# Optimization experiments

Hardware: AMD Instinct MI355X
Metric: run time of the kernel (lower is better)

The kernel has to match this reference:

```python
import jax, jax.numpy as jnp
import numpy as np

DN = ('NHWC', 'HWIO', 'NHWC')
EPS = 1e-8
BN_EPS = 1e-3
ROUT_ITERS = 3


def _bn(x, p, axis):
    # p: [4, C] rows = gamma, beta, moving_mean, moving_var (inference-mode BN)
    shp = [1] * x.ndim
    shp[axis % x.ndim] = x.shape[axis % x.ndim]
    g, b, m, v = [p[i].reshape(shp) for i in range(4)]
    return (x - m) * jax.lax.rsqrt(v + BN_EPS) * g + b


def _conv(x, w, b, stride, pad):
    return jax.lax.conv_general_dilated(x, w, (stride, stride), pad, dimension_numbers=DN) + b


def _patches(x, k, s):
    # x: [B, H, W, ...] -> [B, Ho, Wo, k*k, ...] (static k*k strided slices, no big gathers)
    Ho = (x.shape[1] - k) // s + 1
    Wo = (x.shape[2] - k) // s + 1
    sl = [x[:, i:i + s * (Ho - 1) + 1:s, j:j + s * (Wo - 1) + 1:s]
          for i in range(k) for j in range(k)]
    return jnp.stack(sl, axis=3)


def _em_routing(votes, a_in, beta_a, beta_u, iters=ROUT_ITERS):
    # votes: [..., Nin, Nout, D], a_in: [..., Nin]; Hinton matrix-capsule EM routing
    Nout = votes.shape[-2]
    R = jnp.full(votes.shape[:-1], 1.0 / Nout, votes.dtype)  # [..., Nin, Nout]
    a_ex = a_in[..., None]
    for i in range(iters):
        lam = 0.01 * (i + 1)  # inverse-temperature schedule
        Ra = R * a_ex                                             # [..., Nin, Nout]
        Rs = Ra.sum(-2) + EPS                                     # [..., Nout]
        mu = jnp.einsum('...no,...nod->...od', Ra, votes) / Rs[..., None]
        diff2 = (votes - mu[..., None, :, :]) ** 2                # [..., Nin, Nout, D]
        sig2 = jnp.einsum('...no,...nod->...od', Ra, diff2) / Rs[..., None] + EPS
        cost = (beta_u[:, None] + 0.5 * jnp.log(sig2)) * Rs[..., None]
        a_out = jax.nn.sigmoid(lam * (beta_a - cost.sum(-1)))     # [..., Nout]
        if i < iters - 1:
            logp = -0.5 * jnp.sum(diff2 / sig2[..., None, :, :]
                                  + jnp.log(2.0 * jnp.pi * sig2)[..., None, :, :], axis=-1)
            R = jax.nn.softmax(jnp.log(a_out + EPS)[..., None, :] + logp, axis=-1)
    return mu, a_out


def _convcaps(pose, a, W, beta_a, beta_u, k=3, s=2):
    # pose: [B,H,W,C,4,4], a: [B,H,W,C]; W: [k*k*C, Cout, 4, 4]
    pp = _patches(pose, k, s)                  # [B,Ho,Wo,k*k,C,4,4]
    B, Ho, Wo = pp.shape[:3]
    pp = pp.reshape(B, Ho, Wo, -1, 4, 4)       # [B,Ho,Wo,Nin,4,4]
    ap = _patches(a, k, s).reshape(B, Ho, Wo, -1)
    Cout = W.shape[1]
    votes = jnp.einsum('bhwnij,nojk->bhwnoik', pp, W).reshape(B, Ho, Wo, pp.shape[3], Cout, 16)
    mu, a_out = _em_routing(votes, ap, beta_a, beta_u)
    return mu.reshape(B, Ho, Wo, Cout, 4, 4), a_out


def reference(x, conv_w, conv_b, bn1, prim_pose_w, prim_pose_b, prim_act_w, prim_act_b,
              bn2, cc1_w, cc1_ba, cc1_bu, bn3, cc2_w, cc2_ba, cc2_bu, bn4,
              dc_w, dc_ba, dc_bu, dec_w1, dec_b1, dec_w2, dec_b2, dec_w3, dec_b3):
    h = jax.nn.relu(_conv(x, conv_w, conv_b, 2, 'SAME'))          # conv1 + relu
    h = _bn(h, bn1, -1)
    pose = _conv(h, prim_pose_w, prim_pose_b, 2, 'VALID')         # PrimaryCaps pose conv
    B, H, W, _ = pose.shape
    pose = pose.reshape(B, H, W, 32, 4, 4)
    a = jax.nn.sigmoid(_conv(h, prim_act_w, prim_act_b, 2, 'VALID'))
    pose = _bn(pose, bn2, -3)
    pose, a = _convcaps(pose, a, cc1_w, cc1_ba, cc1_bu)
    pose = _bn(pose, bn3, -3)
    pose, a = _convcaps(pose, a, cc2_w, cc2_ba, cc2_bu)
    pose = _bn(pose, bn4, -3)
    # DenseCaps: flatten spatial grid of capsules
    pflat = pose.reshape(B, -1, 4, 4)                             # [B, 1152, 4, 4]
    aflat = a.reshape(B, -1)
    votes = jnp.einsum('bnij,nojk->bnoik', pflat, dc_w).reshape(B, pflat.shape[1], dc_w.shape[1], 16)
    mu, a_out = _em_routing(votes, aflat, dc_ba, dc_bu)           # mu: [B, 32, 16]
    dec_in = mu.reshape(B, -1)                                    # [B, 512]
    h = jax.nn.relu(dec_in @ dec_w1 + dec_b1)
    h = jax.nn.relu(h @ dec_w2 + dec_b2)
    return h @ dec_w3 + dec_b3


def _bn_params(k, C):
    k1, k2, k3, k4 = jax.random.split(k, 4)
    return jnp.stack([1.0 + 0.05 * jax.random.normal(k1, (C,)),
                      0.05 * jax.random.normal(k2, (C,)),
                      0.01 * jax.random.normal(k3, (C,)),
                      1.0 + 0.1 * jax.random.uniform(k4, (C,))]).astype(jnp.float32)


def setup_inputs() -> dict:
    key = jax.random.key(0)
    ks = jax.random.split(key, 24)
    B, HW, NV = 2, 128, 8192
    n = lambda k, s, sc: (sc * jax.random.normal(k, s)).astype(jnp.float32)
    return {
        'x': n(ks[0], (B, HW, HW, 3), 1.0),
        'conv_w': n(ks[1], (11, 11, 3, 96), 0.05), 'conv_b': n(ks[2], (96,), 0.05),
        'bn1': _bn_params(ks[3], 96),
        'prim_pose_w': n(ks[4], (9, 9, 96, 32 * 16), 0.05), 'prim_pose_b': n(ks[5], (32 * 16,), 0.05),
        'prim_act_w': n(ks[6], (9, 9, 96, 32), 0.05), 'prim_act_b': n(ks[7], (32,), 0.05),
        'bn2': _bn_params(ks[8], 32),
        'cc1_w': n(ks[9], (3 * 3 * 32, 32, 4, 4), 0.1),
        'cc1_ba': n(ks[10], (32,), 0.5), 'cc1_bu': n(ks[11], (32,), 0.5),
        'bn3': _bn_params(ks[12], 32),
        'cc2_w': n(ks[13], (3 * 3 * 32, 32, 4, 4), 0.1),
        'cc2_ba': n(ks[14], (32,), 0.5), 'cc2_bu': n(ks[15], (32,), 0.5),
        'bn4': _bn_params(ks[16], 32),
        'dc_w': n(ks[17], (6 * 6 * 32, 32, 4, 4), 0.1),
        'dc_ba': n(ks[18], (32,), 0.5), 'dc_bu': n(ks[19], (32,), 0.5),
        'dec_w1': n(ks[20], (512, 512), 0.05), 'dec_b1': jnp.zeros((512,), jnp.float32),
        'dec_w2': n(ks[21], (512, 1024), 0.05), 'dec_b2': jnp.zeros((1024,), jnp.float32),
        'dec_w3': n(ks[22], (1024, NV), 0.02), 'dec_b3': jnp.zeros((NV,), jnp.float32),
    }
```

## Files before the change

### kernel.cpp

```cpp
#include <hip/hip_runtime.h>
#include <hip/hip_bf16.h>

#define EPSR 1e-8f
#define BNEPS 1e-3f
#define LOG2PI 1.8378770664093453f

#define O_H      0
#define O_POSE2  786432
#define O_ACT2   1589248
#define O_POSE3  1639424
#define O_ACT3   1812480
#define O_POSE4  1823296
#define O_ACT4   1860160
#define O_DECIN  1862464
#define O_H1     1863488
#define O_H2     1864512
#define O_PART   1866560
#define O_DSTAT  0
#define O_DCOMB  32768

__global__ __launch_bounds__(256) void conv1_k(
    const float* __restrict__ x, const float* __restrict__ w,
    const float* __restrict__ bias, const float* __restrict__ bn1,
    float* __restrict__ h)
{
  int t = blockIdx.x * 256 + threadIdx.x;
  int c = t % 96; int px = t / 96;
  int ox = px & 63; int r = px >> 6; int oy = r & 63; int b = r >> 6;
  float acc = 0.f;
  int iy0 = 2*oy - 4, ix0 = 2*ox - 4;
  for (int ky = 0; ky < 11; ++ky) {
    int iy = iy0 + ky;
    if ((unsigned)iy > 127u) continue;
    const float* xrow = x + (size_t)((b*128 + iy)*128)*3;
    const float* wrow = w + (ky*11*3)*96 + c;
    for (int kx = 0; kx < 11; ++kx) {
      int ix = ix0 + kx;
      if ((unsigned)ix > 127u) continue;
      const float* xp = xrow + ix*3;
      const float* wp = wrow + kx*3*96;
      acc = fmaf(xp[0], wp[0],   acc);
      acc = fmaf(xp[1], wp[96],  acc);
      acc = fmaf(xp[2], wp[192], acc);
    }
  }
  acc += bias[c];
  acc = fmaxf(acc, 0.f);
  float g = bn1[c], be = bn1[96+c], mm = bn1[192+c], vv = bn1[288+c];
  h[t] = (acc - mm) * (g * rsqrtf(vv + BNEPS)) + be;
}

__global__ __launch_bounds__(256) void zero_raw(float* __restrict__ pose2, float* __restrict__ act2)
{
  int t = blockIdx.x * 256 + threadIdx.x;
  if (t < 802816) pose2[t] = 0.f;
  else act2[t - 802816] = 0.f;
}

__global__ __launch_bounds__(256) void conv2_gemm_ks(
    const float* __restrict__ h,
    const float* __restrict__ pw, const float* __restrict__ aw,
    float* __restrict__ pose2r, float* __restrict__ act2r)
{
  __shared__ float As[2][16][68];
  __shared__ float Bs[2][16][68];
  const int tid = threadIdx.x;
  const int mb = blockIdx.x, nb = blockIdx.y, z = blockIdx.z;
  const int m0 = mb * 64;
  const float* Bp; int ldB, n0;
  if (nb < 8) { Bp = pw; ldB = 512; n0 = nb * 64; } else { Bp = aw; ldB = 32; n0 = 0; }

  const int a_ml = tid & 63, a_cig = tid >> 6;
  const int am = m0 + a_ml;
  const bool am_ok = am < 1568;
  int ab_ = am / 784; int ayx = am - ab_*784;
  int aoy = ayx / 28, aox = ayx - aoy*28;
  if (!am_ok) { ab_ = 0; aoy = 0; aox = 0; }
  const float* a_base = h + (size_t)((ab_*64 + 2*aoy)*64 + 2*aox)*96 + a_cig*4;

  const int b_kk = tid >> 4, b_ng = tid & 15;
  const int b_col = b_ng * 4;
  const bool b_ok = b_col < ldB;

  const int tm = (tid & 15) * 4, tn = (tid >> 4) * 4;
  float acc[4][4] = {{0}};

  auto kidx = [](int kt, int& ky, int& kx, int& ci0) {
    int cig = kt % 6; int r = kt / 6; kx = r % 9; ky = r / 9; ci0 = cig * 16;
  };
  auto ldAv = [&](int ky, int kx, int ci0) -> float4 {
    if (!am_ok) return make_float4(0,0,0,0);
    return *(const float4*)(a_base + (ky*64 + kx)*96 + ci0);
  };
  auto ldBv = [&](int kt) -> float4 {
    if (!b_ok) return make_float4(0,0,0,0);
    return *(const float4*)(Bp + (size_t)(kt*16 + b_kk) * ldB + n0 + b_col);
  };
  auto wrAv = [&](float4 v, int buf) {
    As[buf][a_cig*4+0][a_ml] = v.x;
    As[buf][a_cig*4+1][a_ml] = v.y;
    As[buf][a_cig*4+2][a_ml] = v.z;
    As[buf][a_cig*4+3][a_ml] = v.w;
  };
  auto wrBv = [&](float4 v, int buf) {
    *(float4*)&Bs[buf][b_kk][b_col] = v;
  };

  const int kt0 = z * 81;
  {
    int ky, kx, ci0; kidx(kt0, ky, kx, ci0);
    wrAv(ldAv(ky, kx, ci0), 0); wrBv(ldBv(kt0), 0);
  }
  __syncthreads();

  for (int i = 0; i < 81; ++i) {
    int cur = i & 1;
    bool st = i < 80;
    float4 va, vb;
    if (st) {
      int ky, kx, ci0; kidx(kt0 + i + 1, ky, kx, ci0);
      va = ldAv(ky, kx, ci0);
      vb = ldBv(kt0 + i + 1);
    }
    #pragma unroll
    for (int kk = 0; kk < 16; ++kk) {
      float4 av = *(const float4*)&As[cur][kk][tm];
      float4 bv = *(const float4*)&Bs[cur][kk][tn];
      float aa[4] = {av.x, av.y, av.z, av.w};
      float bb4[4] = {bv.x, bv.y, bv.z, bv.w};
      #pragma unroll
      for (int ii = 0; ii < 4; ++ii)
        #pragma unroll
        for (int jj = 0; jj < 4; ++jj)
          acc[ii][jj] = fmaf(aa[ii], bb4[jj], acc[ii][jj]);
    }
    if (st) { wrAv(va, cur ^ 1); wrBv(vb, cur ^ 1); }
    __syncthreads();
  }

  #pragma unroll
  for (int i = 0; i < 4; ++i) {
    int m = m0 + tm + i;
    if (m >= 1568) break;
    #pragma unroll
    for (int j = 0; j < 4; ++j) {
      int nl = tn + j;
      if (nb < 8) {
        atomicAdd(&pose2r[(size_t)m*512 + n0 + nl], acc[i][j]);
      } else if (nl < 32) {
        atomicAdd(&act2r[(size_t)m*32 + nl], acc[i][j]);
      }
    }
  }
}

__global__ __launch_bounds__(256) void conv2_epi(
    const float* __restrict__ pb, const float* __restrict__ ab,
    const float* __restrict__ bn2,
    float* __restrict__ pose2, float* __restrict__ act2)
{
  int t = blockIdx.x * 256 + threadIdx.x;
  if (t < 802816) {
    int n = t & 511;
    float val = pose2[t] + pb[n];
    int caps = n >> 4;
    float g = bn2[caps], be = bn2[32+caps], mm = bn2[64+caps], vv = bn2[96+caps];
    pose2[t] = (val - mm) * (g * rsqrtf(vv + BNEPS)) + be;
  } else {
    int t2 = t - 802816;
    int nl = t2 & 31;
    float val = act2[t2] + ab[nl];
    act2[t2] = 1.f / (1.f + expf(-val));
  }
}

template<int NIN, int NWAVES, bool CONV>
__global__ __launch_bounds__(NWAVES*64) void routing_k(
    const float* __restrict__ pose_in, const float* __restrict__ act_in,
    const float* __restrict__ Wv,
    const float* __restrict__ ba, const float* __restrict__ bu,
    const float* __restrict__ bn,
    float* __restrict__ pose_out, float* __restrict__ act_out,
    int Hin, int Win, int Wout)
{
  constexpr int NT  = NWAVES * 64;
  constexpr int NPW = NIN / NWAVES;
  __shared__ float s1s[NWAVES][32*17];
  __shared__ float s2s[NWAVES][32*17];
  __shared__ float rsP[NWAVES][32];
  __shared__ float muS[32*17], isgS[32*17], lgS[32*17];
  __shared__ float laS[32], lsS[32], aoS[32], RsS[32], S0S[32];

  const int tid = threadIdx.x;
  const int wv = tid >> 6, lane = tid & 63;
  const int o = lane & 31, half = lane >> 5;

  int bb = 0, oy = 0, ox = 0;
  if (CONV) {
    int px = blockIdx.x;
    ox = px % Wout; int t2 = px / Wout; oy = t2 % Wout; bb = t2 / Wout;
  } else {
    bb = blockIdx.x;
  }

  float mur[8], isgr[8], lar = 0.f, lsr = 0.f;
  #pragma unroll
  for (int i = 0; i < 8; ++i) { mur[i] = 0.f; isgr[i] = 0.f; }

  for (int p = 0; p < 3; ++p) {
    float lam = 0.01f * (float)(p + 1);
    float s1r[8] = {0,0,0,0,0,0,0,0};
    float s2r[8] = {0,0,0,0,0,0,0,0};
    float rsr = 0.f;

    for (int it = 0; it < NPW; ++it) {
      int n = wv * NPW + it;
      const float* wp = Wv + (size_t)(n*32 + o) * 16;
      float4 w0 = *(const float4*)(wp);
      float4 w1 = *(const float4*)(wp + 4);
      float4 w2 = *(const float4*)(wp + 8);
      float4 w3 = *(const float4*)(wp + 12);
      const float* pp; float an;
      if (CONV) {
        int c = n & 31, kk = n >> 5;
        int ki = kk / 3, kj = kk - ki*3;
        int pix = (bb*Hin + 2*oy + ki)*Win + 2*ox + kj;
        pp = pose_in + (size_t)(pix*32 + c) * 16;
        an = act_in[pix*32 + c];
      } else {
        pp = pose_in + (size_t)(bb*NIN + n) * 16;
        an = act_in[bb*NIN + n];
      }
      float4 p0 = *(const float4*)(pp + half*8);
      float4 p1 = *(const float4*)(pp + half*8 + 4);
      float v[8];
      v[0] = fmaf(p0.x,w0.x, fmaf(p0.y,w1.x, fmaf(p0.z,w2.x, p0.w*w3.x)));
      v[1] = fmaf(p0.x,w0.y, fmaf(p0.y,w1.y, fmaf(p0.z,w2.y, p0.w*w3.y)));
      v[2] = fmaf(p0.x,w0.z, fmaf(p0.y,w1.z, fmaf(p0.z,w2.z, p0.w*w3.z)));
      v[3] = fmaf(p0.x,w0.w, fmaf(p0.y,w1.w, fmaf(p0.z,w2.w, p0.w*w3.w)));
      v[4] = fmaf(p1.x,w0.x, fmaf(p1.y,w1.x, fmaf(p1.z,w2.x, p1.w*w3.x)));
      v[5] = fmaf(p1.x,w0.y, fmaf(p1.y,w1.y, fmaf(p1.z,w2.y, p1.w*w3.y)));
      v[6] = fmaf(p1.x,w0.z, fmaf(p1.y,w1.z, fmaf(p1.z,w2.z, p1.w*w3.z)));
      v[7] = fmaf(p1.x,w0.w, fmaf(p1.y,w1.w, fmaf(p1.z,w2.w, p1.w*w3.w)));

      float R;
      if (p == 0) {
        R = 1.f / 32.f;
      } else {
        float t = 0.f;
        #pragma unroll
        for (int dd = 0; dd < 8; ++dd) { float df = v[dd] - mur[dd]; t = fmaf(df*df, isgr[dd], t); }
        t += __shfl_xor(t, 32, 64);
        float logit = lar - 0.5f * (t + lsr);
        float mx = logit;
        mx = fmaxf(mx, __shfl_xor(mx, 16, 64));
        mx = fmaxf(mx, __shfl_xor(mx,  8, 64));
        mx = fmaxf(mx, __shfl_xor(mx,  4, 64));
        mx = fmaxf(mx, __shfl_xor(mx,  2, 64));
        mx = fmaxf(mx, __shfl_xor(mx,  1, 64));
        float e = expf(logit - mx);
        float se = e;
        se += __shfl_xor(se, 16, 64);
        se += __shfl_xor(se,  8, 64);
        se += __shfl_xor(se,  4, 64);
        se += __shfl_xor(se,  2, 64);
        se += __shfl_xor(se,  1, 64);
        R = e / se;
      }
      float Ra = R * an;
      rsr += Ra;
      #pragma unroll
      for (int dd = 0; dd < 8; ++dd) {
        s1r[dd] = fmaf(Ra, v[dd], s1r[dd]);
        s2r[dd] = fmaf(Ra * v[dd], v[dd], s2r[dd]);
      }
    }

    #pragma unroll
    for (int dd = 0; dd < 8; ++dd) {
      s1s[wv][o*17 + half*8 + dd] = s1r[dd];
      s2s[wv][o*17 + half*8 + dd] = s2r[dd];
    }
    if (!half) rsP[wv][o] = rsr;
    __syncthreads();
    if (tid < 32) {
      float r = 0.f;
      #pragma unroll
      for (int w2 = 0; w2 < NWAVES; ++w2) r += rsP[w2][tid];
      S0S[tid] = r; RsS[tid] = r + EPSR;
    }
    __syncthreads();
    for (int idx = tid; idx < 512; idx += NT) {
      int oo = idx >> 4, d = idx & 15;
      float S1 = 0.f, S2 = 0.f;
      #pragma unroll
      for (int w2 = 0; w2 < NWAVES; ++w2) { S1 += s1s[w2][oo*17+d]; S2 += s2s[w2][oo*17+d]; }
      float Rs = RsS[oo];
      float m_ = S1 / Rs;
      float sg = (S2 - 2.f*m_*S1 + m_*m_*S0S[oo]) / Rs + EPSR;
      muS[oo*17+d]  = m_;
      isgS[oo*17+d] = 1.f / sg;
      lgS[oo*17+d]  = logf(sg);
    }
    __syncthreads();
    if (tid < 32) {
      float L = 0.f;
      #pragma unroll
      for (int d = 0; d < 16; ++d) L += lgS[tid*17 + d];
      float cost = (16.f*bu[tid] + 0.5f*L) * RsS[tid];
      float av = 1.f / (1.f + expf(-lam * (ba[tid] - cost)));
      aoS[tid] = av;
      laS[tid] = logf(av + EPSR);
      lsS[tid] = 16.f*LOG2PI + L;
    }
    __syncthreads();
    if (p < 2) {
      #pragma unroll
      for (int dd = 0; dd < 8; ++dd) {
        mur[dd]  = muS[o*17 + half*8 + dd];
        isgr[dd] = isgS[o*17 + half*8 + dd];
      }
      lar = laS[o]; lsr = lsS[o];
    }
  }

  if (CONV) {
    int pxo = (bb*Wout + oy)*Wout + ox;
    for (int idx = tid; idx < 512; idx += NT) {
      int oo = idx >> 4, d = idx & 15;
      float val = muS[oo*17 + d];
      float g = bn[oo], be = bn[32+oo], mm = bn[64+oo], vv = bn[96+oo];
      val = (val - mm) * (g * rsqrtf(vv + BNEPS)) + be;
      pose_out[(size_t)pxo*512 + idx] = val;
    }
    if (tid < 32) act_out[(size_t)pxo*32 + tid] = aoS[tid];
  } else {
    for (int idx = tid; idx < 512; idx += NT)
      pose_out[(size_t)bb*512 + idx] = muS[(idx>>4)*17 + (idx&15)];
  }
}

template<int P>
__global__ __launch_bounds__(256) void dense_stats(
    const float* __restrict__ pose_in, const float* __restrict__ act_in,
    const float* __restrict__ Wv, const float* __restrict__ comb,
    float* __restrict__ stat)
{
  __shared__ float s1s[4][32*17];
  __shared__ float s2s[4][32*17];
  __shared__ float rsP[4][32];
  const int tid = threadIdx.x;
  const int wv = tid >> 6, lane = tid & 63;
  const int o = lane & 31, half = lane >> 5;
  const int bb = blockIdx.x / 12, chunk = blockIdx.x % 12;

  float mur[8], isgr[8], lar = 0.f, lsr = 0.f;
  if (P > 0) {
    const float* cb = comb + (size_t)bb * 1088;
    #pragma unroll
    for (int dd = 0; dd < 8; ++dd) {
      mur[dd]  = cb[o*16 + half*8 + dd];
      isgr[dd] = cb[512 + o*16 + half*8 + dd];
    }
    lar = cb[1024 + o]; lsr = cb[1056 + o];
  }

  float s1r[8] = {0,0,0,0,0,0,0,0};
  float s2r[8] = {0,0,0,0,0,0,0,0};
  float rsr = 0.f;

  for (int it = 0; it < 24; ++it) {
    int n = chunk*96 + wv*24 + it;
    const float* wp = Wv + (size_t)(n*32 + o) * 16;
    float4 w0 = *(const float4*)(wp);
    float4 w1 = *(const float4*)(wp + 4);
    float4 w2 = *(const float4*)(wp + 8);
    float4 w3 = *(const float4*)(wp + 12);
    const float* pp = pose_in + (size_t)(bb*1152 + n) * 16;
    float an = act_in[bb*1152 + n];
    float4 p0 = *(const float4*)(pp + half*8);
    float4 p1 = *(const float4*)(pp + half*8 + 4);
    float v[8];
    v[0] = fmaf(p0.x,w0.x, fmaf(p0.y,w1.x, fmaf(p0.z,w2.x, p0.w*w3.x)));
    v[1] = fmaf(p0.x,w0.y, fmaf(p0.y,w1.y, fmaf(p0.z,w2.y, p0.w*w3.y)));
    v[2] = fmaf(p0.x,w0.z, fmaf(p0.y,w1.z, fmaf(p0.z,w2.z, p0.w*w3.z)));
    v[3] = fmaf(p0.x,w0.w, fmaf(p0.y,w1.w, fmaf(p0.z,w2.w, p0.w*w3.w)));
    v[4] = fmaf(p1.x,w0.x, fmaf(p1.y,w1.x, fmaf(p1.z,w2.x, p1.w*w3.x)));
    v[5] = fmaf(p1.x,w0.y, fmaf(p1.y,w1.y, fmaf(p1.z,w2.y, p1.w*w3.y)));
    v[6] = fmaf(p1.x,w0.z, fmaf(p1.y,w1.z, fmaf(p1.z,w2.z, p1.w*w3.z)));
    v[7] = fmaf(p1.x,w0.w, fmaf(p1.y,w1.w, fmaf(p1.z,w2.w, p1.w*w3.w)));

    float R;
    if (P == 0) {
      R = 1.f / 32.f;
    } else {
      float t = 0.f;
      #pragma unroll
      for (int dd = 0; dd < 8; ++dd) { float df = v[dd] - mur[dd]; t = fmaf(df*df, isgr[dd], t); }
      t += __shfl_xor(t, 32, 64);
      float logit = lar - 0.5f * (t + lsr);
      float mx = logit;
      mx = fmaxf(mx, __shfl_xor(mx, 16, 64));
      mx = fmaxf(mx, __shfl_xor(mx,  8, 64));
      mx = fmaxf(mx, __shfl_xor(mx,  4, 64));
      mx = fmaxf(mx, __shfl_xor(mx,  2, 64));
      mx = fmaxf(mx, __shfl_xor(mx,  1, 64));
      float e = expf(logit - mx);
      float se = e;
      se += __shfl_xor(se, 16, 64);
      se += __shfl_xor(se,  8, 64);
      se += __shfl_xor(se,  4, 64);
      se += __shfl_xor(se,  2, 64);
      se += __shfl_xor(se,  1, 64);
      R = e / se;
    }
    float Ra = R * an;
    rsr += Ra;
    #pragma unroll
    for (int dd = 0; dd < 8; ++dd) {
      s1r[dd] = fmaf(Ra, v[dd], s1r[dd]);
      s2r[dd] = fmaf(Ra * v[dd], v[dd], s2r[dd]);
    }
  }

  #pragma unroll
  for (int dd = 0; dd < 8; ++dd) {
    s1s[wv][o*17 + half*8 + dd] = s1r[dd];
    s2s[wv][o*17 + half*8 + dd] = s2r[dd];
  }
  if (!half) rsP[wv][o] = rsr;
  __syncthreads();

  float* out = stat + (size_t)(bb*12 + chunk) * 1056;
  for (int idx = tid; idx < 512; idx += 256) {
    int oo = idx >> 4, d = idx & 15;
    float S1 = 0.f, S2 = 0.f;
    #pragma unroll
    for (int w2 = 0; w2 < 4; ++w2) { S1 += s1s[w2][oo*17+d]; S2 += s2s[w2][oo*17+d]; }
    out[idx] = S1; out[512 + idx] = S2;
  }
  if (tid < 32) {
    float r = 0.f;
    #pragma unroll
    for (int w2 = 0; w2 < 4; ++w2) r += rsP[w2][tid];
    out[1024 + tid] = r;
  }
}

template<int P>
__global__ __launch_bounds__(256) void dense_comb(
    const float* __restrict__ stat,
    const float* __restrict__ ba, const float* __restrict__ bu,
    float* __restrict__ comb, float* __restrict__ decin)
{
  __shared__ float S0S[32], RsS[32], lgS[32*17];
  const int tid = threadIdx.x;
  const int bb = blockIdx.x;
  const float* st = stat + (size_t)bb * 12 * 1056;
  float* cb = comb + (size_t)bb * 1088;

  if (tid < 32) {
    float r = 0.f;
    #pragma unroll
    for (int c = 0; c < 12; ++c) r += st[c*1056 + 1024 + tid];
    S0S[tid] = r; RsS[tid] = r + EPSR;
  }
  __syncthreads();
  for (int idx = tid; idx < 512; idx += 256) {
    int oo = idx >> 4, d = idx & 15;
    float S1 = 0.f, S2 = 0.f;
    #pragma unroll
    for (int c = 0; c < 12; ++c) { S1 += st[c*1056 + idx]; S2 += st[c*1056 + 512 + idx]; }
    float Rs = RsS[oo];
    float m_ = S1 / Rs;
    float sg = (S2 - 2.f*m_*S1 + m_*m_*S0S[oo]) / Rs + EPSR;
    if (P == 2) {
      decin[(size_t)bb*512 + idx] = m_;
    } else {
      cb[idx] = m_;
      cb[512 + idx] = 1.f / sg;
    }
    lgS[oo*17 + d] = logf(sg);
  }
  __syncthreads();
  if (P < 2 && tid < 32) {
    float L = 0.f;
    #pragma unroll
    for (int d = 0; d < 16; ++d) L += lgS[tid*17 + d];
    float lam = 0.01f * (float)(P + 1);
    float cost = (16.f*bu[tid] + 0.5f*L) * RsS[tid];
    float av = 1.f / (1.f + expf(-lam * (ba[tid] - cost)));
    cb[1024 + tid] = logf(av + EPSR);
    cb[1056 + tid] = 16.f*LOG2PI + L;
  }
}

__global__ __launch_bounds__(256) void fc_partial(
    const float* __restrict__ in, const float* __restrict__ W,
    float* __restrict__ part, int K, int N, int CK)
{
  int t = blockIdx.x * 256 + threadIdx.x;
  int nj = N >> 2;
  int j4 = t % nj, ks = t / nj;
  int k0 = ks * CK;
  float4 a0 = make_float4(0,0,0,0), a1 = make_float4(0,0,0,0);
  const float4* Wp = (const float4*)W;
  for (int kk = 0; kk < CK; ++kk) {
    int k = k0 + kk;
    float4 wv = Wp[(size_t)k * nj + j4];
    float f0 = in[k], f1 = in[K + k];
    a0.x = fmaf(f0, wv.x, a0.x); a0.y = fmaf(f0, wv.y, a0.y);
    a0.z = fmaf(f0, wv.z, a0.z); a0.w = fmaf(f0, wv.w, a0.w);
    a1.x = fmaf(f1, wv.x, a1.x); a1.y = fmaf(f1, wv.y, a1.y);
    a1.z = fmaf(f1, wv.z, a1.z); a1.w = fmaf(f1, wv.w, a1.w);
  }
  ((float4*)part)[(size_t)(ks*2 + 0) * nj + j4] = a0;
  ((float4*)part)[(size_t)(ks*2 + 1) * nj + j4] = a1;
}

__global__ __launch_bounds__(256) void fc_reduce(
    const float* __restrict__ part, const float* __restrict__ bias,
    float* __restrict__ out, int N, int KS, int relu)
{
  int t = blockIdx.x * 256 + threadIdx.x;
  int b = t / N, j = t - b*N;
  float s = bias[j];
  for (int ks = 0; ks < KS; ++ks) s += part[(size_t)(ks*2 + b) * N + j];
  if (relu) s = fmaxf(s, 0.f);
  out[(size_t)b*N + j] = s;
}

extern "C" void kernel_launch(void* const* d_in, const int* in_sizes, int n_in,
                              void* d_out, int out_size, void* d_ws, size_t ws_size,
                              hipStream_t stream) {
  const float* x    = (const float*)d_in[0];
  const float* c1w  = (const float*)d_in[1];
  const float* c1b  = (const float*)d_in[2];
  const float* bn1  = (const float*)d_in[3];
  const float* ppw  = (const float*)d_in[4];
  const float* ppb  = (const float*)d_in[5];
  const float* paw  = (const float*)d_in[6];
  const float* pab  = (const float*)d_in[7];
  const float* bn2  = (const float*)d_in[8];
  const float* ccw1 = (const float*)d_in[9];
  const float* cba1 = (const float*)d_in[10];
  const float* cbu1 = (const float*)d_in[11];
  const float* bn3  = (const float*)d_in[12];
  const float* ccw2 = (const float*)d_in[13];
  const float* cba2 = (const float*)d_in[14];
  const float* cbu2 = (const float*)d_in[15];
  const float* bn4  = (const float*)d_in[16];
  const float* dcw  = (const float*)d_in[17];
  const float* dcba = (const float*)d_in[18];
  const float* dcbu = (const float*)d_in[19];
  const float* w1   = (const float*)d_in[20];
  const float* b1   = (const float*)d_in[21];
  const float* w2   = (const float*)d_in[22];
  const float* b2   = (const float*)d_in[23];
  const float* w3   = (const float*)d_in[24];
  const float* b3   = (const float*)d_in[25];

  float* ws    = (float*)d_ws;
  float* h     = ws + O_H;
  float* pose2 = ws + O_POSE2;
  float* act2  = ws + O_ACT2;
  float* pose3 = ws + O_POSE3;
  float* act3  = ws + O_ACT3;
  float* pose4 = ws + O_POSE4;
  float* act4  = ws + O_ACT4;
  float* decin = ws + O_DECIN;
  float* h1    = ws + O_H1;
  float* h2    = ws + O_H2;
  float* part  = ws + O_PART;
  float* dstat = ws + O_DSTAT;
  float* dcomb = ws + O_DCOMB;

  conv1_k<<<3072, 256, 0, stream>>>(x, c1w, c1b, bn1, h);
  zero_raw<<<3332, 256, 0, stream>>>(pose2, act2);
  conv2_gemm_ks<<<dim3(25, 9, 6), 256, 0, stream>>>(h, ppw, paw, pose2, act2);
  conv2_epi<<<3332, 256, 0, stream>>>(ppb, pab, bn2, pose2, act2);
  routing_k<288, 8, true><<<338, 512, 0, stream>>>(pose2, act2, ccw1, cba1, cbu1, bn3,
                                                   pose3, act3, 28, 28, 13);
  routing_k<288, 8, true><<<72, 512, 0, stream>>>(pose3, act3, ccw2, cba2, cbu2, bn4,
                                                  pose4, act4, 13, 13, 6);
  dense_stats<0><<<24, 256, 0, stream>>>(pose4, act4, dcw, nullptr, dstat);
  dense_comb<0><<<2, 256, 0, stream>>>(dstat, dcba, dcbu, dcomb, nullptr);
  dense_stats<1><<<24, 256, 0, stream>>>(pose4, act4, dcw, dcomb, dstat);
  dense_comb<1><<<2, 256, 0, stream>>>(dstat, dcba, dcbu, dcomb, nullptr);
  dense_stats<2><<<24, 256, 0, stream>>>(pose4, act4, dcw, dcomb, dstat);
  dense_comb<2><<<2, 256, 0, stream>>>(dstat, dcba, dcbu, dcomb, decin);
  fc_partial<<<8, 256, 0, stream>>>(decin, w1, part, 512, 512, 32);
  fc_reduce<<<4, 256, 0, stream>>>(part, b1, h1, 512, 16, 1);
  fc_partial<<<16, 256, 0, stream>>>(h1, w2, part, 512, 1024, 32);
  fc_reduce<<<8, 256, 0, stream>>>(part, b2, h2, 1024, 16, 1);
  fc_partial<<<64, 256, 0, stream>>>(h2, w3, part, 1024, 8192, 128);
  fc_reduce<<<64, 256, 0, stream>>>(part, b3, (float*)d_out, 8192, 8, 0);
}
```

Before: 825.5 us.

## Run primary-capsule conv GEMM on MFMA with split-fp16 hi/lo emulation

```diff
diff --git a/kernel.cpp b/kernel.cpp
--- a/kernel.cpp
+++ b/kernel.cpp
@@ -4,6 +4,11 @@
 #define EPSR 1e-8f
 #define BNEPS 1e-3f
 #define LOG2PI 1.8378770664093453f
+
+typedef _Float16 f16;
+typedef _Float16 f16x4 __attribute__((ext_vector_type(4)));
+typedef _Float16 f16x8 __attribute__((ext_vector_type(8)));
+typedef float f32x4 __attribute__((ext_vector_type(4)));
 
 #define O_H      0
 #define O_POSE2  786432
@@ -16,13 +21,17 @@
 #define O_H1     1863488
 #define O_H2     1864512
 #define O_PART   1866560
+#define O_BWH    1997632
+#define O_BWL    4485952
+#define NEED_BYTES (6974272ull * 4ull)
 #define O_DSTAT  0
 #define O_DCOMB  32768
 
+template<int F16>
 __global__ __launch_bounds__(256) void conv1_k(
     const float* __restrict__ x, const float* __restrict__ w,
     const float* __restrict__ bias, const float* __restrict__ bn1,
-    float* __restrict__ h)
+    float* __restrict__ h32, f16* __restrict__ hh, f16* __restrict__ hl)
 {
   int t = blockIdx.x * 256 + threadIdx.x;
   int c = t % 96; int px = t / 96;
@@ -47,7 +56,42 @@
   acc += bias[c];
   acc = fmaxf(acc, 0.f);
   float g = bn1[c], be = bn1[96+c], mm = bn1[192+c], vv = bn1[288+c];
-  h[t] = (acc - mm) * (g * rsqrtf(vv + BNEPS)) + be;
+  float val = (acc - mm) * (g * rsqrtf(vv + BNEPS)) + be;
+  if (F16) {
+    f16 hi = (f16)val;
+    f16 lo = (f16)(val - (float)hi);
+    hh[t] = hi; hl[t] = lo;
+  } else {
+    h32[t] = val;
+  }
+}
+
+__global__ __launch_bounds__(256) void split_w_k(
+    const float* __restrict__ pw, const float* __restrict__ aw,
+    f16* __restrict__ bwh, f16* __restrict__ bwl)
+{
+  __shared__ float tile[32][33];
+  const int kb = blockIdx.x * 32, nb = blockIdx.y * 32;
+  const int t = threadIdx.x;
+  #pragma unroll
+  for (int p = 0; p < 4; ++p) {
+    int k_l = p*8 + (t>>5), n_l = t & 31;
+    int k = kb + k_l, n = nb + n_l;
+    float v = 0.f;
+    if (n < 512) v = pw[(size_t)k*512 + n];
+    else if (n < 544) v = aw[(size_t)k*32 + (n - 512)];
+    tile[k_l][n_l] = v;
+  }
+  __syncthreads();
+  #pragma unroll
+  for (int p = 0; p < 4; ++p) {
+    int n_l = p*8 + (t>>5), k_l = t & 31;
+    float v = tile[k_l][n_l];
+    f16 hi = (f16)v;
+    f16 lo = (f16)(v - (float)hi);
+    size_t dst = (size_t)(nb + n_l)*7776 + kb + k_l;
+    bwh[dst] = hi; bwl[dst] = lo;
+  }
 }
 
 __global__ __launch_bounds__(256) void zero_raw(float* __restrict__ pose2, float* __restrict__ act2)
@@ -55,6 +99,129 @@
   int t = blockIdx.x * 256 + threadIdx.x;
   if (t < 802816) pose2[t] = 0.f;
   else act2[t - 802816] = 0.f;
+}
+
+__global__ __launch_bounds__(256, 2) void conv2_mfma(
+    const f16* __restrict__ hh, const f16* __restrict__ hl,
+    const f16* __restrict__ bwh, const f16* __restrict__ bwl,
+    float* __restrict__ pose2r, float* __restrict__ act2r)
+{
+  __shared__ f16 Ah[128*32];
+  __shared__ f16 Al[128*32];
+  __shared__ f16 Bh[128*32];
+  __shared__ f16 Bl[128*32];
+  const int tid = threadIdx.x;
+  const int mb = blockIdx.x, nb = blockIdx.y, z = blockIdx.z;
+  const int m0 = mb*128, n0 = nb*128;
+  const int q = 243 / 8, rch = 243 % 8;
+  const int k0 = z*q + (z < rch ? z : rch);
+  const int k1 = k0 + q + (z < rch ? 1 : 0);
+
+  const int srow = tid >> 3;
+  const int c    = tid & 7;
+  int habase[4]; bool amok[4];
+  #pragma unroll
+  for (int p = 0; p < 4; ++p) {
+    int m = m0 + p*32 + srow;
+    amok[p] = m < 1568;
+    int mm = amok[p] ? m : 0;
+    int b = mm / 784; int yx = mm - b*784; int oy = yx / 28, ox = yx - oy*28;
+    habase[p] = ((b*64 + 2*oy)*64 + 2*ox)*96;
+  }
+  size_t bbase[4];
+  #pragma unroll
+  for (int p = 0; p < 4; ++p) bbase[p] = (size_t)(n0 + p*32 + srow) * 7776;
+
+  f16x4 rah[4], ral[4], rbh[4], rbl[4];
+  const f16x4 zv = {(f16)0, (f16)0, (f16)0, (f16)0};
+
+  auto load_step = [&](int kt) {
+    int ky = kt / 27, rr = kt % 27; int kx = rr / 3, ci0 = (rr % 3) * 32;
+    int aoff = (ky*64 + kx)*96 + ci0 + c*4;
+    int koff = kt*32 + c*4;
+    #pragma unroll
+    for (int p = 0; p < 4; ++p) {
+      if (amok[p]) {
+        rah[p] = *(const f16x4*)(hh + habase[p] + aoff);
+        ral[p] = *(const f16x4*)(hl + habase[p] + aoff);
+      } else { rah[p] = zv; ral[p] = zv; }
+      rbh[p] = *(const f16x4*)(bwh + bbase[p] + koff);
+      rbl[p] = *(const f16x4*)(bwl + bbase[p] + koff);
+    }
+  };
+
+  int widx[4];
+  #pragma unroll
+  for (int p = 0; p < 4; ++p) {
+    int row = p*32 + srow;
+    widx[p] = row*32 + ((((c>>1) + (row>>1)) & 3) << 3) + ((c & 1) << 2);
+  }
+
+  const int wv = tid >> 6, lane = tid & 63;
+  const int wr = wv >> 1, wc = wv & 1;
+  const int l15 = lane & 15, g = lane >> 4;
+
+  f32x4 acc[4][4];
+  #pragma unroll
+  for (int i = 0; i < 4; ++i)
+    #pragma unroll
+    for (int j = 0; j < 4; ++j) acc[i][j] = (f32x4){0.f, 0.f, 0.f, 0.f};
+
+  int aidx[4], bidx[4];
+  #pragma unroll
+  for (int i = 0; i < 4; ++i) {
+    int arow = wr*64 + i*16 + l15;
+    aidx[i] = arow*32 + (((g + (arow>>1)) & 3) << 3);
+    int brow = wc*64 + i*16 + l15;
+    bidx[i] = brow*32 + (((g + (brow>>1)) & 3) << 3);
+  }
+
+  load_step(k0);
+  for (int kt = k0; kt < k1; ++kt) {
+    __syncthreads();
+    #pragma unroll
+    for (int p = 0; p < 4; ++p) {
+      *(f16x4*)&Ah[widx[p]] = rah[p];
+      *(f16x4*)&Al[widx[p]] = ral[p];
+      *(f16x4*)&Bh[widx[p]] = rbh[p];
+      *(f16x4*)&Bl[widx[p]] = rbl[p];
+    }
+    __syncthreads();
+    if (kt + 1 < k1) load_step(kt + 1);
+    f16x8 ah[4], al[4], bh[4], bl[4];
+    #pragma unroll
+    for (int i = 0; i < 4; ++i) {
+      ah[i] = *(const f16x8*)&Ah[aidx[i]];
+      al[i] = *(const f16x8*)&Al[aidx[i]];
+      bh[i] = *(const f16x8*)&Bh[bidx[i]];
+      bl[i] = *(const f16x8*)&Bl[bidx[i]];
+    }
+    #pragma unroll
+    for (int i = 0; i < 4; ++i)
+      #pragma unroll
+      for (int j = 0; j < 4; ++j) {
+        acc[i][j] = __builtin_amdgcn_mfma_f32_16x16x32_f16(ah[i], bh[j], acc[i][j], 0, 0, 0);
+        acc[i][j] = __builtin_amdgcn_mfma_f32_16x16x32_f16(ah[i], bl[j], acc[i][j], 0, 0, 0);
+        acc[i][j] = __builtin_amdgcn_mfma_f32_16x16x32_f16(al[i], bh[j], acc[i][j], 0, 0, 0);
+      }
+  }
+
+  #pragma unroll
+  for (int i = 0; i < 4; ++i) {
+    #pragma unroll
+    for (int j = 0; j < 4; ++j) {
+      #pragma unroll
+      for (int r2 = 0; r2 < 4; ++r2) {
+        int m = m0 + wr*64 + i*16 + g*4 + r2;
+        int n = n0 + wc*64 + j*16 + l15;
+        if (m < 1568) {
+          float val = acc[i][j][r2];
+          if (n < 512) atomicAdd(&pose2r[(size_t)m*512 + n], val);
+          else if (n < 544) atomicAdd(&act2r[(size_t)m*32 + (n - 512)], val);
+        }
+      }
+    }
+  }
 }
 
 __global__ __launch_bounds__(256) void conv2_gemm_ks(
@@ -222,11 +389,11 @@
       float4 w3 = *(const float4*)(wp + 12);
       const float* pp; float an;
       if (CONV) {
-        int c = n & 31, kk = n >> 5;
+        int cc = n & 31, kk = n >> 5;
         int ki = kk / 3, kj = kk - ki*3;
         int pix = (bb*Hin + 2*oy + ki)*Win + 2*ox + kj;
-        pp = pose_in + (size_t)(pix*32 + c) * 16;
-        an = act_in[pix*32 + c];
+        pp = pose_in + (size_t)(pix*32 + cc) * 16;
+        an = act_in[pix*32 + cc];
       } else {
         pp = pose_in + (size_t)(bb*NIN + n) * 16;
         an = act_in[bb*NIN + n];
@@ -562,6 +729,8 @@
 
   float* ws    = (float*)d_ws;
   float* h     = ws + O_H;
+  f16*   hh    = (f16*)(ws + O_H);
+  f16*   hl    = hh + 786432;
   float* pose2 = ws + O_POSE2;
   float* act2  = ws + O_ACT2;
   float* pose3 = ws + O_POSE3;
@@ -572,12 +741,23 @@
   float* h1    = ws + O_H1;
   float* h2    = ws + O_H2;
   float* part  = ws + O_PART;
+  f16*   bwh   = (f16*)(ws + O_BWH);
+  f16*   bwl   = (f16*)(ws + O_BWL);
   float* dstat = ws + O_DSTAT;
   float* dcomb = ws + O_DCOMB;
 
-  conv1_k<<<3072, 256, 0, stream>>>(x, c1w, c1b, bn1, h);
-  zero_raw<<<3332, 256, 0, stream>>>(pose2, act2);
-  conv2_gemm_ks<<<dim3(25, 9, 6), 256, 0, stream>>>(h, ppw, paw, pose2, act2);
+  const bool fast = ws_size >= NEED_BYTES;
+
+  if (fast) {
+    conv1_k<1><<<3072, 256, 0, stream>>>(x, c1w, c1b, bn1, nullptr, hh, hl);
+    split_w_k<<<dim3(243, 20), 256, 0, stream>>>(ppw, paw, bwh, bwl);
+    zero_raw<<<3332, 256, 0, stream>>>(pose2, act2);
+    conv2_mfma<<<dim3(13, 5, 8), 256, 0, stream>>>(hh, hl, bwh, bwl, pose2, act2);
+  } else {
+    conv1_k<0><<<3072, 256, 0, stream>>>(x, c1w, c1b, bn1, h, nullptr, nullptr);
+    zero_raw<<<3332, 256, 0, stream>>>(pose2, act2);
+    conv2_gemm_ks<<<dim3(25, 9, 6), 256, 0, stream>>>(h, ppw, paw, pose2, act2);
+  }
   conv2_epi<<<3332, 256, 0, stream>>>(ppb, pab, bn2, pose2, act2);
   routing_k<288, 8, true><<<338, 512, 0, stream>>>(pose2, act2, ccw1, cba1, cbu1, bn3,
                                                    pose3, act3, 28, 28, 13);
```

Result: faster. 696.7 us (-15.6%).
